# Optimization experiments

Measured on AMD Instinct MI355X. Metric: run time of the kernel, lower is better.

The kernel has to match this reference:

```python
import jax, jax.numpy as jnp
import numpy as np
import math

HEAD_DIM = 128
N_HEADS_Q = 32
N_KV_HEADS = 8
N_REP = N_HEADS_Q // N_KV_HEADS
ROPE_BASE = 10000.0


def _rope(x, start_pos):
    # x: [b, s, h, d] -- rotate interleaved pairs, Llama-style
    b, s, h, d = x.shape
    pos = start_pos + jnp.arange(s, dtype=jnp.float32)            # [s]
    inv_freq = 1.0 / (ROPE_BASE ** (jnp.arange(0, d, 2, dtype=jnp.float32) / d))  # [d/2]
    ang = pos[:, None] * inv_freq[None, :]                         # [s, d/2]
    cos = jnp.cos(ang)[None, :, None, :].astype(x.dtype)
    sin = jnp.sin(ang)[None, :, None, :].astype(x.dtype)
    x1 = x[..., 0::2]
    x2 = x[..., 1::2]
    out = jnp.stack([x1 * cos - x2 * sin, x1 * sin + x2 * cos], axis=-1)
    return out.reshape(b, s, h, d)


def setup_inputs() -> dict:
    key = jax.random.key(0)
    ks = jax.random.split(key, 5)
    dim = N_HEADS_Q * HEAD_DIM
    kv_dim = N_KV_HEADS * HEAD_DIM
    sc = 0.02
    return {
        "x": jax.random.normal(ks[0], (2, 2048, dim), dtype=jnp.float32),
        "wq": jax.random.normal(ks[1], (dim, dim), dtype=jnp.float32) * sc,
        "wk": jax.random.normal(ks[2], (kv_dim, dim), dtype=jnp.float32) * sc,
        "wv": jax.random.normal(ks[3], (kv_dim, dim), dtype=jnp.float32) * sc,
        "wo": jax.random.normal(ks[4], (dim, dim), dtype=jnp.float32) * sc,
        "start_pos": 0,
    }


def reference(x, wq, wk, wv, wo, start_pos):
    b, s, dim = x.shape
    # QKV projections (nn.Linear: y = x @ W.T)
    xq = (x @ wq.T).reshape(b, s, N_HEADS_Q, HEAD_DIM)
    xk = (x @ wk.T).reshape(b, s, N_KV_HEADS, HEAD_DIM)
    xv = (x @ wv.T).reshape(b, s, N_KV_HEADS, HEAD_DIM)
    xq = _rope(xq, start_pos)
    xk = _rope(xk, start_pos)
    # KV cache: start_pos=0 prefill -> cached prefix == freshly written xk/xv
    keys, values = xk, xv
    # GQA attention without materializing repeated KV:
    # q grouped as [b, q, n_kv, n_rep, d]
    qg = xq.reshape(b, s, N_KV_HEADS, N_REP, HEAD_DIM)
    scores = jnp.einsum("bqhrd,bkhd->bhrqk", qg, keys) / math.sqrt(HEAD_DIM)
    probs = jax.nn.softmax(scores, axis=-1)  # no causal mask in original
    out = jnp.einsum("bhrqk,bkhd->bqhrd", probs, values)
    out = out.reshape(b, s, N_HEADS_Q * HEAD_DIM)
    return out @ wo.T
```

## Files before the change

kernel.cpp:

```cpp
#include <hip/hip_runtime.h>
#include <cstdint>
#include <cstddef>

typedef _Float16 f16x8 __attribute__((ext_vector_type(8)));
typedef _Float16 f16x4 __attribute__((ext_vector_type(4)));
typedef _Float16 f16x2 __attribute__((ext_vector_type(2)));
typedef float    f32x4 __attribute__((ext_vector_type(4)));

__device__ __forceinline__ void async16(const void* g, void* l) {
  __builtin_amdgcn_global_load_lds(
      (const __attribute__((address_space(1))) void*)g,
      (__attribute__((address_space(3))) void*)l, 16, 0, 0);
}

__global__ void cvt_kernel(const float* __restrict__ in, _Float16* __restrict__ out, int n4) {
  int i = blockIdx.x * blockDim.x + threadIdx.x;
  int stride = gridDim.x * blockDim.x;
  for (; i < n4; i += stride) {
    float4 f = ((const float4*)in)[i];
    f16x4 o;
    o[0] = (_Float16)f.x; o[1] = (_Float16)f.y;
    o[2] = (_Float16)f.z; o[3] = (_Float16)f.w;
    ((f16x4*)out)[i] = o;
  }
}

__global__ void rope_kernel(_Float16* __restrict__ X, const int* __restrict__ sp,
                            int ppShift, int sMask, int nPairs) {
  int i = blockIdx.x * blockDim.x + threadIdx.x;
  int stride = gridDim.x * blockDim.x;
  int start = *sp;
  for (int p = i; p < nPairs; p += stride) {
    int row = p >> ppShift;
    int pc  = p & ((1 << ppShift) - 1);
    int fi  = pc & 63;
    int s   = row & sMask;
    float ang = (float)(start + s) * exp2f(-0.20762050593046014f * (float)fi);
    float sn, cs;
    __sincosf(ang, &sn, &cs);
    uint32_t u = ((uint32_t*)X)[p];
    f16x2 v = __builtin_bit_cast(f16x2, u);
    float x1 = (float)v[0], x2 = (float)v[1];
    v[0] = (_Float16)(x1 * cs - x2 * sn);
    v[1] = (_Float16)(x1 * sn + x2 * cs);
    ((uint32_t*)X)[p] = __builtin_bit_cast(uint32_t, v);
  }
}

template<int OUT_MODE>
__global__ __launch_bounds__(256, 3)
void gemm_nt(const _Float16* __restrict__ A, const _Float16* __restrict__ B,
             void* __restrict__ Cp, void* __restrict__ Cp2,
             int M, int N, int K) {
  __shared__ __align__(16) _Float16 As[128 * 64];
  __shared__ __align__(16) _Float16 Bs[128 * 64];
  const int tid  = threadIdx.x;
  const int wave = tid >> 6, lane = tid & 63;
  const int l15  = lane & 15, quad = lane >> 4;
  const int m0 = blockIdx.y * 128, n0 = blockIdx.x * 128;
  const int wm = (wave >> 1) * 64, wn = (wave & 1) * 64;
  f32x4 acc[4][4] = {};
  const int cbase = wave * 256;

  for (int kb = 0; kb < K; kb += 64) {
    #pragma unroll
    for (int i = 0; i < 4; ++i) {
      int base = cbase + i * 64;
      int idx  = base + lane;
      int row  = idx >> 3, pos = idx & 7;
      int c    = pos ^ (row & 7);
      async16(A + (size_t)(m0 + row) * K + kb + c * 8, (char*)As + base * 16);
      async16(B + (size_t)(n0 + row) * K + kb + c * 8, (char*)Bs + base * 16);
    }
    __syncthreads();
    #pragma unroll
    for (int ks = 0; ks < 2; ++ks) {
      f16x8 af[4], bfv[4];
      #pragma unroll
      for (int t = 0; t < 4; ++t) {
        int ra = wm + t * 16 + l15;
        int pa = (ks * 4 + quad) ^ (ra & 7);
        af[t] = *(const f16x8*)((const char*)As + ra * 128 + pa * 16);
        int rb = wn + t * 16 + l15;
        int pb = (ks * 4 + quad) ^ (rb & 7);
        bfv[t] = *(const f16x8*)((const char*)Bs + rb * 128 + pb * 16);
      }
      #pragma unroll
      for (int mt = 0; mt < 4; ++mt)
        #pragma unroll
        for (int nt = 0; nt < 4; ++nt)
          acc[mt][nt] = __builtin_amdgcn_mfma_f32_16x16x32_f16(af[mt], bfv[nt], acc[mt][nt], 0, 0, 0);
    }
    __syncthreads();
  }

  if constexpr (OUT_MODE == 0) {
    _Float16* Cb = (_Float16*)Cp;
    #pragma unroll
    for (int mt = 0; mt < 4; ++mt)
      #pragma unroll
      for (int r = 0; r < 4; ++r) {
        size_t row = (size_t)(m0 + wm + mt * 16 + quad * 4 + r);
        #pragma unroll
        for (int nt = 0; nt < 4; ++nt)
          Cb[row * N + n0 + wn + nt * 16 + l15] = (_Float16)acc[mt][nt][r];
      }
  } else if constexpr (OUT_MODE == 2) {
    float* Cf = (float*)Cp;
    #pragma unroll
    for (int mt = 0; mt < 4; ++mt)
      #pragma unroll
      for (int r = 0; r < 4; ++r) {
        size_t row = (size_t)(m0 + wm + mt * 16 + quad * 4 + r);
        #pragma unroll
        for (int nt = 0; nt < 4; ++nt)
          Cf[row * N + n0 + wn + nt * 16 + l15] = acc[mt][nt][r];
      }
  } else if constexpr (OUT_MODE == 3) {
    const int half = N >> 1;
    if (n0 < half) {
      _Float16* Cb = (_Float16*)Cp;
      #pragma unroll
      for (int mt = 0; mt < 4; ++mt)
        #pragma unroll
        for (int r = 0; r < 4; ++r) {
          size_t row = (size_t)(m0 + wm + mt * 16 + quad * 4 + r);
          #pragma unroll
          for (int nt = 0; nt < 4; ++nt)
            Cb[row * half + n0 + wn + nt * 16 + l15] = (_Float16)acc[mt][nt][r];
        }
    } else {
      _Float16* Ct = (_Float16*)Cp2;
      #pragma unroll
      for (int mt = 0; mt < 4; ++mt)
        #pragma unroll
        for (int nt = 0; nt < 4; ++nt) {
          size_t crow = (size_t)(n0 - half + wn + nt * 16 + l15);
          size_t ccol = (size_t)(m0 + wm + mt * 16 + quad * 4);
          f16x4 t;
          t[0] = (_Float16)acc[mt][nt][0]; t[1] = (_Float16)acc[mt][nt][1];
          t[2] = (_Float16)acc[mt][nt][2]; t[3] = (_Float16)acc[mt][nt][3];
          *(f16x4*)(Ct + crow * M + ccol) = t;
        }
    }
  }
}

__global__ __launch_bounds__(256, 2)
void flash_kernel(const _Float16* __restrict__ Q, const _Float16* __restrict__ Kg,
                  const _Float16* __restrict__ Vt, _Float16* __restrict__ O,
                  int S, int T) {
  __shared__ __align__(16) _Float16 Kt[2][64 * 128];
  __shared__ __align__(16) _Float16 Vs[2][128 * 64];
  __shared__ __align__(16) _Float16 Ps[4 * 32 * 64];
  const int tid  = threadIdx.x;
  const int wave = tid >> 6, lane = tid & 63;
  const int l15  = lane & 15, quad = lane >> 4;
  const int qt = blockIdx.x, hq = blockIdx.y, b = blockIdx.z;
  const int kvh = hq >> 2;
  const float scale = 0.12751744f;

  f16x8 qf[2][4];
  #pragma unroll
  for (int mt = 0; mt < 2; ++mt)
    #pragma unroll
    for (int ks = 0; ks < 4; ++ks) {
      size_t row = (size_t)b * S + qt * 128 + wave * 32 + mt * 16 + l15;
      qf[mt][ks] = *(const f16x8*)(Q + row * 4096 + hq * 128 + ks * 32 + quad * 8);
    }

  f32x4 oacc[2][8] = {};
  float mi[2][4], li[2][4];
  #pragma unroll
  for (int mt = 0; mt < 2; ++mt)
    #pragma unroll
    for (int r = 0; r < 4; ++r) { mi[mt][r] = -1e30f; li[mt][r] = 0.f; }

  const int nkt = S >> 6;

  auto stage = [&](int kt, int buf) {
    #pragma unroll
    for (int i = 0; i < 4; ++i) {
      int base = wave * 256 + i * 64;
      int idx  = base + lane;
      { int row = idx >> 4, pos = idx & 15, c = pos ^ (row & 15);
        async16(Kg + (size_t)(b * S + kt * 64 + row) * 1024 + kvh * 128 + c * 8,
                (char*)Kt[buf] + base * 16); }
      { int row = idx >> 3, pos = idx & 7, c = pos ^ (row & 7);
        async16(Vt + (size_t)(kvh * 128 + row) * T + b * S + kt * 64 + c * 8,
                (char*)Vs[buf] + base * 16); }
    }
  };

  stage(0, 0);
  __syncthreads();
  int cur = 0;

  for (int kt = 0; kt < nkt; ++kt) {
    if (kt + 1 < nkt) stage(kt + 1, cur ^ 1);

    f32x4 sacc[2][4] = {};
    #pragma unroll
    for (int ks = 0; ks < 4; ++ks) {
      f16x8 kf[4];
      #pragma unroll
      for (int nt = 0; nt < 4; ++nt) {
        int rk = nt * 16 + l15;
        int pp = (ks * 4 + quad) ^ (rk & 15);
        kf[nt] = *(const f16x8*)((const char*)Kt[cur] + rk * 256 + pp * 16);
      }
      __builtin_amdgcn_s_setprio(1);
      #pragma unroll
      for (int mt = 0; mt < 2; ++mt)
        #pragma unroll
        for (int nt = 0; nt < 4; ++nt)
          sacc[mt][nt] = __builtin_amdgcn_mfma_f32_16x16x32_f16(qf[mt][ks], kf[nt], sacc[mt][nt], 0, 0, 0);
      __builtin_amdgcn_s_setprio(0);
    }

    #pragma unroll
    for (int mt = 0; mt < 2; ++mt) {
      float mx[4];
      #pragma unroll
      for (int r = 0; r < 4; ++r)
        mx[r] = fmaxf(fmaxf(sacc[mt][0][r], sacc[mt][1][r]),
                      fmaxf(sacc[mt][2][r], sacc[mt][3][r]));
      #pragma unroll
      for (int d = 1; d < 16; d <<= 1)
        #pragma unroll
        for (int r = 0; r < 4; ++r)
          mx[r] = fmaxf(mx[r], __shfl_xor(mx[r], d));
      bool grow = false;
      #pragma unroll
      for (int r = 0; r < 4; ++r) grow = grow || (mx[r] > mi[mt][r] + 24.0f);
      if (__any(grow)) {
        #pragma unroll
        for (int r = 0; r < 4; ++r) {
          float mnew = fmaxf(mi[mt][r], mx[r]);
          float al = exp2f((mi[mt][r] - mnew) * scale);
          mi[mt][r] = mnew;
          li[mt][r] *= al;
          #pragma unroll
          for (int nt = 0; nt < 8; ++nt) oacc[mt][nt][r] *= al;
        }
      }
      float nm[4], rs[4];
      #pragma unroll
      for (int r = 0; r < 4; ++r) { nm[r] = -mi[mt][r] * scale; rs[r] = 0.f; }
      #pragma unroll
      for (int nt = 0; nt < 4; ++nt)
        #pragma unroll
        for (int r = 0; r < 4; ++r) {
          float p = exp2f(fmaf(sacc[mt][nt][r], scale, nm[r]));
          sacc[mt][nt][r] = p;
          rs[r] += p;
        }
      #pragma unroll
      for (int d = 1; d < 16; d <<= 1)
        #pragma unroll
        for (int r = 0; r < 4; ++r)
          rs[r] += __shfl_xor(rs[r], d);
      #pragma unroll
      for (int r = 0; r < 4; ++r)
        li[mt][r] += rs[r];
      #pragma unroll
      for (int nt = 0; nt < 4; ++nt)
        #pragma unroll
        for (int r = 0; r < 4; ++r) {
          int prow = mt * 16 + quad * 4 + r;
          int key  = nt * 16 + l15;
          int pos  = (key >> 3) ^ (prow & 7);
          Ps[wave * 2048 + prow * 64 + pos * 8 + (key & 7)] = (_Float16)sacc[mt][nt][r];
        }
    }

    #pragma unroll
    for (int k2 = 0; k2 < 2; ++k2) {
      f16x8 pf[2], vf[8];
      #pragma unroll
      for (int mt = 0; mt < 2; ++mt) {
        int rp = mt * 16 + l15;
        int pp = (k2 * 4 + quad) ^ (rp & 7);
        pf[mt] = *(const f16x8*)((const char*)Ps + wave * 4096 + rp * 128 + pp * 16);
      }
      #pragma unroll
      for (int nt = 0; nt < 8; ++nt) {
        int rv = nt * 16 + l15;
        int pp = (k2 * 4 + quad) ^ (rv & 7);
        vf[nt] = *(const f16x8*)((const char*)Vs[cur] + rv * 128 + pp * 16);
      }
      __builtin_amdgcn_s_setprio(1);
      #pragma unroll
      for (int mt = 0; mt < 2; ++mt)
        #pragma unroll
        for (int nt = 0; nt < 8; ++nt)
          oacc[mt][nt] = __builtin_amdgcn_mfma_f32_16x16x32_f16(pf[mt], vf[nt], oacc[mt][nt], 0, 0, 0);
      __builtin_amdgcn_s_setprio(0);
    }

    __syncthreads();
    cur ^= 1;
  }

  #pragma unroll
  for (int mt = 0; mt < 2; ++mt)
    #pragma unroll
    for (int r = 0; r < 4; ++r) {
      float inv = 1.0f / li[mt][r];
      size_t row = (size_t)b * S + qt * 128 + wave * 32 + mt * 16 + quad * 4 + r;
      #pragma unroll
      for (int nt = 0; nt < 8; ++nt)
        O[row * 4096 + hq * 128 + nt * 16 + l15] = (_Float16)(oacc[mt][nt][r] * inv);
    }
}

extern "C" void kernel_launch(void* const* d_in, const int* in_sizes, int n_in,
                              void* d_out, int out_size, void* d_ws, size_t ws_size,
                              hipStream_t stream) {
  const float* x  = (const float*)d_in[0];
  const float* wq = (const float*)d_in[1];
  const float* wk = (const float*)d_in[2];
  const float* wv = (const float*)d_in[3];
  const float* wo = (const float*)d_in[4];
  const int*   sp = (const int*)d_in[5];

  const int dim = 4096, kvdim = 1024;
  const int T = in_sizes[0] / dim;
  const int B = 2;
  const int S = T / B;

  _Float16* xb   = (_Float16*)d_ws;
  _Float16* wqb  = xb   + (size_t)T * dim;
  _Float16* wkvb = wqb  + (size_t)dim * dim;
  _Float16* wob  = wkvb + (size_t)2 * kvdim * dim;
  _Float16* XQ   = wob  + (size_t)dim * dim;
  _Float16* XK   = XQ   + (size_t)T * dim;
  _Float16* VT   = XK   + (size_t)T * kvdim;
  _Float16* AO   = xb;

  auto cvt = [&](const float* src, _Float16* dst, size_t n) {
    int n4 = (int)(n / 4);
    int blocks = (n4 + 255) / 256;
    if (blocks > 4096) blocks = 4096;
    cvt_kernel<<<blocks, 256, 0, stream>>>(src, dst, n4);
  };
  cvt(x,  xb,  (size_t)T * dim);
  cvt(wq, wqb, (size_t)dim * dim);
  cvt(wk, wkvb, (size_t)kvdim * dim);
  cvt(wv, wkvb + (size_t)kvdim * dim, (size_t)kvdim * dim);
  cvt(wo, wob, (size_t)dim * dim);

  gemm_nt<0><<<dim3(dim / 128, T / 128), 256, 0, stream>>>(xb, wqb, XQ, nullptr, T, dim, dim);
  gemm_nt<3><<<dim3((2 * kvdim) / 128, T / 128), 256, 0, stream>>>(xb, wkvb, XK, VT, T, 2 * kvdim, dim);

  rope_kernel<<<4096, 256, 0, stream>>>(XQ, sp, 11, S - 1, T * dim / 2);
  rope_kernel<<<2048, 256, 0, stream>>>(XK, sp,  9, S - 1, T * kvdim / 2);

  flash_kernel<<<dim3(S / 128, 32, B), 256, 0, stream>>>(XQ, XK, VT, AO, S, T);

  gemm_nt<2><<<dim3(dim / 128, T / 128), 256, 0, stream>>>(AO, wob, d_out, nullptr, T, dim, dim);
}
```

Baseline: 888.2 us.

## Single-buffer K/V with split staging, raise occupancy, and compute row sums via MFMA

The flash attention kernel drops double-buffered K/V shared memory in favour of single buffers. The next K tile is loaded after the QK^T phase and the next V tile after the PV phase, so each load overlaps the other phase's compute. The smaller shared-memory footprint allows `__launch_bounds__` to request 3 blocks per SM instead of 2. The softmax row sum is now accumulated by an extra MFMA against a vector of ones instead of a shuffle reduction, and the PV loop is restructured per row tile. The risks are an extra barrier per iteration, less latency hiding than true double buffering, and possible register pressure from the tighter launch bound.

```diff
diff --git a/kernel.cpp b/kernel.cpp
--- a/kernel.cpp
+++ b/kernel.cpp
@@ -146,12 +146,12 @@
   }
 }
 
-__global__ __launch_bounds__(256, 2)
+__global__ __launch_bounds__(256, 3)
 void flash_kernel(const _Float16* __restrict__ Q, const _Float16* __restrict__ Kg,
                   const _Float16* __restrict__ Vt, _Float16* __restrict__ O,
                   int S, int T) {
-  __shared__ __align__(16) _Float16 Kt[2][64 * 128];
-  __shared__ __align__(16) _Float16 Vs[2][128 * 64];
+  __shared__ __align__(16) _Float16 Kt[64 * 128];
+  __shared__ __align__(16) _Float16 Vs[128 * 64];
   __shared__ __align__(16) _Float16 Ps[4 * 32 * 64];
   const int tid  = threadIdx.x;
   const int wave = tid >> 6, lane = tid & 63;
@@ -169,36 +169,44 @@
       qf[mt][ks] = *(const f16x8*)(Q + row * 4096 + hq * 128 + ks * 32 + quad * 8);
     }
 
+  const f16x8 ones = {(_Float16)1, (_Float16)1, (_Float16)1, (_Float16)1,
+                      (_Float16)1, (_Float16)1, (_Float16)1, (_Float16)1};
+
   f32x4 oacc[2][8] = {};
-  float mi[2][4], li[2][4];
+  f32x4 liacc[2] = {};
+  float mi[2][4];
   #pragma unroll
   for (int mt = 0; mt < 2; ++mt)
     #pragma unroll
-    for (int r = 0; r < 4; ++r) { mi[mt][r] = -1e30f; li[mt][r] = 0.f; }
+    for (int r = 0; r < 4; ++r) mi[mt][r] = -1e30f;
 
   const int nkt = S >> 6;
 
-  auto stage = [&](int kt, int buf) {
+  auto stageK = [&](int kt) {
     #pragma unroll
     for (int i = 0; i < 4; ++i) {
       int base = wave * 256 + i * 64;
       int idx  = base + lane;
-      { int row = idx >> 4, pos = idx & 15, c = pos ^ (row & 15);
-        async16(Kg + (size_t)(b * S + kt * 64 + row) * 1024 + kvh * 128 + c * 8,
-                (char*)Kt[buf] + base * 16); }
-      { int row = idx >> 3, pos = idx & 7, c = pos ^ (row & 7);
-        async16(Vt + (size_t)(kvh * 128 + row) * T + b * S + kt * 64 + c * 8,
-                (char*)Vs[buf] + base * 16); }
+      int row = idx >> 4, pos = idx & 15, c = pos ^ (row & 15);
+      async16(Kg + (size_t)(b * S + kt * 64 + row) * 1024 + kvh * 128 + c * 8,
+              (char*)Kt + base * 16);
     }
   };
-
-  stage(0, 0);
+  auto stageV = [&](int kt) {
+    #pragma unroll
+    for (int i = 0; i < 4; ++i) {
+      int base = wave * 256 + i * 64;
+      int idx  = base + lane;
+      int row = idx >> 3, pos = idx & 7, c = pos ^ (row & 7);
+      async16(Vt + (size_t)(kvh * 128 + row) * T + b * S + kt * 64 + c * 8,
+              (char*)Vs + base * 16);
+    }
+  };
+
+  stageK(0); stageV(0);
   __syncthreads();
-  int cur = 0;
 
   for (int kt = 0; kt < nkt; ++kt) {
-    if (kt + 1 < nkt) stage(kt + 1, cur ^ 1);
-
     f32x4 sacc[2][4] = {};
     #pragma unroll
     for (int ks = 0; ks < 4; ++ks) {
@@ -207,7 +215,7 @@
       for (int nt = 0; nt < 4; ++nt) {
         int rk = nt * 16 + l15;
         int pp = (ks * 4 + quad) ^ (rk & 15);
-        kf[nt] = *(const f16x8*)((const char*)Kt[cur] + rk * 256 + pp * 16);
+        kf[nt] = *(const f16x8*)((const char*)Kt + rk * 256 + pp * 16);
       }
       __builtin_amdgcn_s_setprio(1);
       #pragma unroll
@@ -217,6 +225,9 @@
           sacc[mt][nt] = __builtin_amdgcn_mfma_f32_16x16x32_f16(qf[mt][ks], kf[nt], sacc[mt][nt], 0, 0, 0);
       __builtin_amdgcn_s_setprio(0);
     }
+
+    __syncthreads();
+    if (kt + 1 < nkt) stageK(kt + 1);
 
     #pragma unroll
     for (int mt = 0; mt < 2; ++mt) {
@@ -239,30 +250,19 @@
           float mnew = fmaxf(mi[mt][r], mx[r]);
           float al = exp2f((mi[mt][r] - mnew) * scale);
           mi[mt][r] = mnew;
-          li[mt][r] *= al;
+          liacc[mt][r] *= al;
           #pragma unroll
           for (int nt = 0; nt < 8; ++nt) oacc[mt][nt][r] *= al;
         }
       }
-      float nm[4], rs[4];
-      #pragma unroll
-      for (int r = 0; r < 4; ++r) { nm[r] = -mi[mt][r] * scale; rs[r] = 0.f; }
+      float nm[4];
+      #pragma unroll
+      for (int r = 0; r < 4; ++r) nm[r] = -mi[mt][r] * scale;
       #pragma unroll
       for (int nt = 0; nt < 4; ++nt)
         #pragma unroll
-        for (int r = 0; r < 4; ++r) {
-          float p = exp2f(fmaf(sacc[mt][nt][r], scale, nm[r]));
-          sacc[mt][nt][r] = p;
-          rs[r] += p;
-        }
-      #pragma unroll
-      for (int d = 1; d < 16; d <<= 1)
-        #pragma unroll
         for (int r = 0; r < 4; ++r)
-          rs[r] += __shfl_xor(rs[r], d);
-      #pragma unroll
-      for (int r = 0; r < 4; ++r)
-        li[mt][r] += rs[r];
+          sacc[mt][nt][r] = exp2f(fmaf(sacc[mt][nt][r], scale, nm[r]));
       #pragma unroll
       for (int nt = 0; nt < 4; ++nt)
         #pragma unroll
@@ -272,41 +272,36 @@
           int pos  = (key >> 3) ^ (prow & 7);
           Ps[wave * 2048 + prow * 64 + pos * 8 + (key & 7)] = (_Float16)sacc[mt][nt][r];
         }
-    }
-
-    #pragma unroll
-    for (int k2 = 0; k2 < 2; ++k2) {
-      f16x8 pf[2], vf[8];
-      #pragma unroll
-      for (int mt = 0; mt < 2; ++mt) {
+      #pragma unroll
+      for (int k2 = 0; k2 < 2; ++k2) {
         int rp = mt * 16 + l15;
-        int pp = (k2 * 4 + quad) ^ (rp & 7);
-        pf[mt] = *(const f16x8*)((const char*)Ps + wave * 4096 + rp * 128 + pp * 16);
-      }
-      #pragma unroll
-      for (int nt = 0; nt < 8; ++nt) {
-        int rv = nt * 16 + l15;
-        int pp = (k2 * 4 + quad) ^ (rv & 7);
-        vf[nt] = *(const f16x8*)((const char*)Vs[cur] + rv * 128 + pp * 16);
-      }
-      __builtin_amdgcn_s_setprio(1);
-      #pragma unroll
-      for (int mt = 0; mt < 2; ++mt)
+        int ppp = (k2 * 4 + quad) ^ (rp & 7);
+        f16x8 pf = *(const f16x8*)((const char*)Ps + wave * 4096 + rp * 128 + ppp * 16);
+        f16x8 vf[8];
+        #pragma unroll
+        for (int nt = 0; nt < 8; ++nt) {
+          int rv = nt * 16 + l15;
+          int pv = (k2 * 4 + quad) ^ (rv & 7);
+          vf[nt] = *(const f16x8*)((const char*)Vs + rv * 128 + pv * 16);
+        }
+        __builtin_amdgcn_s_setprio(1);
+        liacc[mt] = __builtin_amdgcn_mfma_f32_16x16x32_f16(pf, ones, liacc[mt], 0, 0, 0);
         #pragma unroll
         for (int nt = 0; nt < 8; ++nt)
-          oacc[mt][nt] = __builtin_amdgcn_mfma_f32_16x16x32_f16(pf[mt], vf[nt], oacc[mt][nt], 0, 0, 0);
-      __builtin_amdgcn_s_setprio(0);
+          oacc[mt][nt] = __builtin_amdgcn_mfma_f32_16x16x32_f16(pf, vf[nt], oacc[mt][nt], 0, 0, 0);
+        __builtin_amdgcn_s_setprio(0);
+      }
     }
 
     __syncthreads();
-    cur ^= 1;
+    if (kt + 1 < nkt) stageV(kt + 1);
   }
 
   #pragma unroll
   for (int mt = 0; mt < 2; ++mt)
     #pragma unroll
     for (int r = 0; r < 4; ++r) {
-      float inv = 1.0f / li[mt][r];
+      float inv = 1.0f / liacc[mt][r];
       size_t row = (size_t)b * S + qt * 128 + wave * 32 + mt * 16 + quad * 4 + r;
       #pragma unroll
       for (int nt = 0; nt < 8; ++nt)
```

Result: slower. 1.666 ms (+87.6%).
